# Performance work log

Measured on AMD Instinct MI355X. Metric: run time of the kernel, lower is better.

The kernel has to match this reference:

```python
import jax, jax.numpy as jnp
import numpy as np

N, IN_C, HID, OUT_C = 4096, 512, 512, 40
E = 131072
N_CLUSTERS, PCA_K, KMEANS_ITERS = 7, 10, 10
EPS = 1e-12


def _linear_params(key, fin, fout):
    k1, k2 = jax.random.split(key)
    lim = 1.0 / np.sqrt(fin)
    W = jax.random.uniform(k1, (fin, fout), jnp.float32, -lim, lim)
    b = jax.random.uniform(k2, (fout,), jnp.float32, -lim, lim)
    return W, b


def setup_inputs() -> dict:
    key = jax.random.key(0)
    ks = jax.random.split(key, 8)
    x = jax.random.normal(ks[0], (N, IN_C), jnp.float32)
    edge_index = jax.random.randint(ks[1], (2, E), 0, N, dtype=jnp.int32)
    y = jax.random.randint(ks[2], (N,), 0, N_CLUSTERS, dtype=jnp.int32)
    W_ego, b_ego = _linear_params(ks[3], IN_C, HID)
    W_cos, b_cos = _linear_params(ks[4], IN_C, HID)
    W_glob, b_glob = _linear_params(ks[5], IN_C, HID)
    W_fc, b_fc = _linear_params(ks[6], HID + IN_C + HID + HID, OUT_C)
    return dict(x=x, W_ego=W_ego, b_ego=b_ego, W_cos=W_cos, b_cos=b_cos,
                W_glob=W_glob, b_glob=b_glob, W_fc=W_fc, b_fc=b_fc,
                edge_index=edge_index, y=y)


def _mp_layer(x, W, b, src, dst):
    # MessagePassingLayer: scatter-add lin(x)[src] at dst, then relu
    h = x @ W + b
    agg = jax.ops.segment_sum(h[src], dst, num_segments=N)
    return jax.nn.relu(agg)


def _dominant_mask(x):
    # Dominant branch: PCA(10) -> KMeans(n_clusters) -> keep nodes with dist <= median.
    # sklearn's randomized KMeans replaced by deterministic Lloyd iterations
    # (init = first N_CLUSTERS rows); whole pipeline is detached in the original.
    xs = jax.lax.stop_gradient(x)
    xc = xs - xs.mean(0, keepdims=True)
    _, _, vt = jnp.linalg.svd(xc, full_matrices=False)
    feats = xc @ vt[:PCA_K].T  # [N, PCA_K]

    def step(c, _):
        d2 = ((feats[:, None, :] - c[None]) ** 2).sum(-1)  # [N, K]
        lab = jnp.argmin(d2, axis=1)
        sums = jax.ops.segment_sum(feats, lab, num_segments=N_CLUSTERS)
        cnt = jax.ops.segment_sum(jnp.ones((N,), jnp.float32), lab, num_segments=N_CLUSTERS)
        newc = jnp.where(cnt[:, None] > 0, sums / jnp.maximum(cnt, 1.0)[:, None], c)
        return newc, None

    centers, _ = jax.lax.scan(step, feats[:N_CLUSTERS], None, length=KMEANS_ITERS)
    d2 = ((feats[:, None, :] - centers[None]) ** 2).sum(-1)
    lab = jnp.argmin(d2, axis=1)
    dist = jnp.linalg.norm(feats - centers[lab], axis=1)
    keep = dist <= jnp.median(dist)
    return jax.lax.stop_gradient(keep.astype(jnp.float32))


def _forward(x, W_ego, b_ego, W_cos, b_cos, W_glob, b_glob, W_fc, b_fc, src, dst):
    # --- ego branch: exact 2-hop (source_to_target) subgraph mean per node ---
    # B[i, j] = 1 iff edge j->i; subset(i) = {i} | 1-hop | 2-hop (set semantics via >0)
    B = jnp.zeros((N, N), jnp.float32).at[dst, src].add(1.0)
    reach = jnp.eye(N, dtype=jnp.float32) + B + B @ B
    Mf = (reach > 0).astype(jnp.float32)
    ego_feats = (Mf @ x) / Mf.sum(1, keepdims=True)

    # --- Dominant branch: zero out far-from-center nodes ---
    keep = _dominant_mask(x)
    cut_enc = x * keep[:, None]

    # --- cosine branch: segment softmax over outgoing edges grouped by src ---
    norm_x = x / jnp.maximum(jnp.linalg.norm(x, axis=1, keepdims=True), EPS)
    sims = (norm_x[src] * norm_x[dst]).sum(-1)  # [E]
    smax = jax.ops.segment_max(sims, src, num_segments=N)
    ex = jnp.exp(sims - smax[src])
    den = jax.ops.segment_sum(ex, src, num_segments=N)
    w = ex / jnp.maximum(den, EPS)[src]
    num = jax.ops.segment_sum(w[:, None] * x[dst], src, num_segments=N)
    wsum = jax.ops.segment_sum(w, src, num_segments=N)
    deg = jax.ops.segment_sum(jnp.ones((E,), jnp.float32), src, num_segments=N)
    cos_feats = jnp.where(deg[:, None] > 0, num / jnp.maximum(wsum, EPS)[:, None], x)

    # --- encoders + head ---
    global_feats = x @ W_glob + b_glob
    ego_enc = _mp_layer(ego_feats, W_ego, b_ego, src, dst)
    cosine_enc = _mp_layer(cos_feats, W_cos, b_cos, src, dst)
    combined = jnp.concatenate([ego_enc, cut_enc, cosine_enc, global_feats], axis=-1)
    return jax.nn.log_softmax(combined @ W_fc + b_fc, axis=1)


def reference(x, W_ego, b_ego, W_cos, b_cos, W_glob, b_glob, W_fc, b_fc, edge_index, y):
    src, dst = edge_index[0], edge_index[1]
    return _forward(x, W_ego, b_ego, W_cos, b_cos, W_glob, b_glob, W_fc, b_fc, src, dst)
```

## Files before the change

### kernel.cpp

```cpp
#include <hip/hip_runtime.h>
#include <hip/hip_cooperative_groups.h>
#include <math.h>

namespace cg = cooperative_groups;

#define NN 4096
#define NC 512
#define NE 131072

typedef __bf16 bf16x8 __attribute__((ext_vector_type(8)));
typedef float f32x4 __attribute__((ext_vector_type(4)));
typedef unsigned short u16x8 __attribute__((ext_vector_type(8)));

__device__ __forceinline__ unsigned short f2b(float f){
  unsigned u = __float_as_uint(f);
  u += 0x7fffu + ((u >> 16) & 1u);
  return (unsigned short)(u >> 16);
}
__device__ __forceinline__ float b2f(unsigned short h){
  return __uint_as_float(((unsigned)h) << 16);
}
__device__ __forceinline__ float wredsum(float v){
  #pragma unroll
  for (int o = 32; o; o >>= 1) v += __shfl_xor(v, o, 64);
  return v;
}
__device__ __forceinline__ float wredmax(float v){
  #pragma unroll
  for (int o = 32; o; o >>= 1) v = fmaxf(v, __shfl_xor(v, o, 64));
  return v;
}

__global__ __launch_bounds__(256) void k_transconv(const float* __restrict__ src, int R, int C,
    unsigned short* __restrict__ dstT, int ldT, unsigned short* __restrict__ dstD){
  __shared__ unsigned short tile[64][65];
  int bc = blockIdx.x * 64, br = blockIdx.y * 64;
  int t = threadIdx.x, lc = t & 63, lr4 = t >> 6;
  for (int j = 0; j < 16; ++j){
    int r = br + lr4*16 + j, c = bc + lc;
    float v = (r < R && c < C) ? src[(size_t)r*C + c] : 0.f;
    unsigned short b = f2b(v);
    tile[lr4*16+j][lc] = b;
    if (dstD && r < R && c < C) dstD[(size_t)r*C + c] = b;
  }
  __syncthreads();
  for (int j = 0; j < 16; ++j){
    int cc = bc + lr4*16 + j, rr = br + lc;
    if (cc < C && rr < R) dstT[(size_t)cc*ldT + rr] = tile[lc][lr4*16+j];
  }
}

__global__ __launch_bounds__(256) void k_transconv3(const float* __restrict__ A,
    const float* __restrict__ B, const float* __restrict__ C,
    unsigned short* __restrict__ TA, unsigned short* __restrict__ TB, unsigned short* __restrict__ TC){
  __shared__ unsigned short tile[64][65];
  const float* src = (blockIdx.z == 0) ? A : ((blockIdx.z == 1) ? B : C);
  unsigned short* dstT = (blockIdx.z == 0) ? TA : ((blockIdx.z == 1) ? TB : TC);
  int bc = blockIdx.x * 64, br = blockIdx.y * 64;
  int t = threadIdx.x, lc = t & 63, lr4 = t >> 6;
  for (int j = 0; j < 16; ++j){
    int r = br + lr4*16 + j, c = bc + lc;
    tile[lr4*16+j][lc] = f2b(src[(size_t)r*512 + c]);
  }
  __syncthreads();
  for (int j = 0; j < 16; ++j){
    int cc = bc + lr4*16 + j, rr = br + lc;
    dstT[(size_t)cc*512 + rr] = tile[lc][lr4*16+j];
  }
}

__global__ __launch_bounds__(256) void k_normx(const float* __restrict__ x, unsigned short* __restrict__ nx){
  int wid = threadIdx.x >> 6, lane = threadIdx.x & 63;
  int row = blockIdx.x*4 + wid;
  const float* xr = x + (size_t)row*NC + lane*8;
  float v[8]; float ss = 0.f;
  #pragma unroll
  for (int j=0;j<8;j++){ v[j] = xr[j]; ss += v[j]*v[j]; }
  ss = wredsum(ss);
  float sc = 1.0f / fmaxf(sqrtf(ss), 1e-12f);
  u16x8 o;
  #pragma unroll
  for (int j=0;j<8;j++) o[j] = f2b(v[j]*sc);
  *(u16x8*)(nx + (size_t)row*NC + lane*8) = o;
}

__global__ void k_count_b1(const int* __restrict__ src, const int* __restrict__ dst,
    int* cin, int* cout, unsigned long long* B1){
  int e = blockIdx.x*256 + threadIdx.x;
  if (e < NE){
    int s = src[e], d = dst[e];
    atomicAdd(&cout[s], 1);
    atomicAdd(&cin[d], 1);
    atomicOr(&B1[(size_t)d*64 + (s>>6)], 1ull << (s & 63));
  }
}
__global__ __launch_bounds__(1024) void k_scan(const int* __restrict__ cnt0, const int* __restrict__ cnt1,
    int* off0, int* off1, int* fill0, int* fill1){
  __shared__ int s[1024];
  int t = threadIdx.x;
  for (int arr = 0; arr < 2; ++arr){
    const int* cnt = arr ? cnt1 : cnt0;
    int* off = arr ? off1 : off0;
    int* fill = arr ? fill1 : fill0;
    int a0 = cnt[t*4], a1 = cnt[t*4+1], a2 = cnt[t*4+2], a3 = cnt[t*4+3];
    int ts = a0+a1+a2+a3;
    s[t] = ts; __syncthreads();
    for (int o = 1; o < 1024; o <<= 1){
      int v = (t >= o) ? s[t-o] : 0; __syncthreads();
      s[t] += v; __syncthreads();
    }
    int ex = s[t] - ts;
    off[t*4] = ex; off[t*4+1] = ex+a0; off[t*4+2] = ex+a0+a1; off[t*4+3] = ex+a0+a1+a2;
    fill[t*4] = ex; fill[t*4+1] = ex+a0; fill[t*4+2] = ex+a0+a1; fill[t*4+3] = ex+a0+a1+a2;
    if (t == 1023) off[4096] = s[1023];
    __syncthreads();
  }
}
__global__ void k_fill(const int* __restrict__ src, const int* __restrict__ dst,
    int* fin, int* fout, int* csr_in, int* csr_out){
  int e = blockIdx.x*256 + threadIdx.x;
  if (e < NE){
    int s = src[e], d = dst[e];
    int pi = atomicAdd(&fin[d], 1);  csr_in[pi] = s;
    int po = atomicAdd(&fout[s], 1); csr_out[po] = d;
  }
}

__global__ __launch_bounds__(256) void k_bits2(const unsigned long long* __restrict__ B1,
    const int* __restrict__ off_in, const int* __restrict__ csr_in,
    unsigned short* __restrict__ Mf, float* __restrict__ rowrecip){
  int wid = threadIdx.x >> 6, lane = threadIdx.x & 63;
  int node = blockIdx.x*4 + wid;
  unsigned long long bits = B1[(size_t)node*64 + lane];
  if (lane == (node >> 6)) bits |= 1ull << (node & 63);
  int beg = off_in[node], end = off_in[node+1];
  for (int e = beg; e < end; ++e){
    int j = csr_in[e];
    bits |= B1[(size_t)j*64 + lane];
  }
  int pc = __popcll(bits);
  #pragma unroll
  for (int o = 32; o; o >>= 1) pc += __shfl_xor(pc, o, 64);
  if (lane == 0) rowrecip[node] = 1.0f / (float)pc;
  unsigned lo = (unsigned)(bits & 0xffffffffull), hi = (unsigned)(bits >> 32);
  unsigned int* Mrow = (unsigned int*)(Mf + (size_t)node*NN);
  for (int k = 0; k < 32; ++k){
    int srcl = 2*k + (lane >> 5);
    unsigned wlo = (unsigned)__shfl((int)lo, srcl, 64);
    unsigned whi = (unsigned)__shfl((int)hi, srcl, 64);
    unsigned long long w2 = ((unsigned long long)whi << 32) | wlo;
    int sh = (lane & 31) * 2;
    unsigned v = (unsigned)((w2 >> sh) & 3ull);
    Mrow[k*64 + lane] = ((v & 1u) ? 0x3F80u : 0u) | ((v & 2u) ? 0x3F800000u : 0u);
  }
}

template<int MODE>
__global__ __launch_bounds__(256) void gemm_bt(
    const unsigned short* __restrict__ A, int lda,
    const unsigned short* __restrict__ BT, int ldb,
    int K, int nstore,
    float* __restrict__ outF, unsigned short* __restrict__ outB, int ldc,
    const float* __restrict__ bias, const float* __restrict__ rowscale){
  __shared__ unsigned short Asm[64*40];
  __shared__ unsigned short Bsm[128*40];
  const int t = threadIdx.x;
  const int lane = t & 63, wid = t >> 6;
  const int wm = wid >> 1, wn = wid & 1;
  const int row0 = blockIdx.x * 64, col0 = blockIdx.y * 128;
  f32x4 acc[2][4];
  #pragma unroll
  for (int a = 0; a < 2; a++)
    #pragma unroll
    for (int b = 0; b < 4; b++){ acc[a][b][0]=0.f; acc[a][b][1]=0.f; acc[a][b][2]=0.f; acc[a][b][3]=0.f; }

  const int ar = t >> 2, as = t & 3;
  const unsigned short* Ap  = A  + (size_t)(row0 + ar)*lda + as*8;
  const unsigned short* Bp0 = BT + (size_t)(col0 + ar)*ldb + as*8;
  const unsigned short* Bp1 = BT + (size_t)(col0 + ar + 64)*ldb + as*8;
  unsigned short* Asd  = &Asm[ar*40 + as*8];
  unsigned short* Bsd0 = &Bsm[ar*40 + as*8];
  unsigned short* Bsd1 = &Bsm[(ar+64)*40 + as*8];

  const int fr = lane & 15, q = lane >> 4;
  const int aoff = (wm*32 + fr)*40 + q*8;
  const int boff = (wn*64 + fr)*40 + q*8;

  for (int k0 = 0; k0 < K; k0 += 32){
    *(u16x8*)Asd  = *(const u16x8*)(Ap  + k0);
    *(u16x8*)Bsd0 = *(const u16x8*)(Bp0 + k0);
    *(u16x8*)Bsd1 = *(const u16x8*)(Bp1 + k0);
    __syncthreads();
    bf16x8 af0 = *(const bf16x8*)&Asm[aoff];
    bf16x8 af1 = *(const bf16x8*)&Asm[aoff + 16*40];
    bf16x8 bfr[4];
    #pragma unroll
    for (int b = 0; b < 4; b++) bfr[b] = *(const bf16x8*)&Bsm[boff + b*16*40];
    #pragma unroll
    for (int b = 0; b < 4; b++){
      acc[0][b] = __builtin_amdgcn_mfma_f32_16x16x32_bf16(af0, bfr[b], acc[0][b], 0, 0, 0);
      acc[1][b] = __builtin_amdgcn_mfma_f32_16x16x32_bf16(af1, bfr[b], acc[1][b], 0, 0, 0);
    }
    __syncthreads();
  }
  #pragma unroll
  for (int a = 0; a < 2; a++){
    const int grow0 = row0 + wm*32 + a*16 + q*4;
    #pragma unroll
    for (int b = 0; b < 4; b++){
      const int gcol = col0 + wn*64 + b*16 + fr;
      if (gcol < nstore){
        #pragma unroll
        for (int r = 0; r < 4; r++){
          const int grow = grow0 + r;
          float v = acc[a][b][r];
          if (MODE == 0){ v *= rowscale[grow]; outB[(size_t)grow*ldc + gcol] = f2b(v); }
          if (MODE == 1){ v += bias[gcol];     outB[(size_t)grow*ldc + gcol] = f2b(v); }
          if (MODE == 2){ v += bias[gcol];     outF[(size_t)grow*ldc + gcol] = v; }
        }
      }
    }
  }
}

__global__ __launch_bounds__(256) void k_cos(const unsigned short* __restrict__ nx,
    const unsigned short* __restrict__ xb,
    const int* __restrict__ off_out, const int* __restrict__ csr_out,
    unsigned short* __restrict__ cosf){
  __shared__ float simsb[4][256];
  int wid = threadIdx.x >> 6, lane = threadIdx.x & 63;
  int node = blockIdx.x*4 + wid;
  float own[8];
  { u16x8 o = *(const u16x8*)(nx + (size_t)node*NC + lane*8);
    #pragma unroll
    for (int j=0;j<8;j++) own[j] = b2f(o[j]); }
  int beg = off_out[node], end = off_out[node+1], deg = end - beg;
  float m = -3.0e38f;
  for (int e = 0; e < deg; ++e){
    int d = csr_out[beg+e];
    u16x8 nb = *(const u16x8*)(nx + (size_t)d*NC + lane*8);
    float sp = 0.f;
    #pragma unroll
    for (int j=0;j<8;j++) sp += own[j]*b2f(nb[j]);
    float s = wredsum(sp);
    if (e < 256 && lane == 0) simsb[wid][e] = s;
    m = fmaxf(m, s);
  }
  float den = 0.f, acc[8] = {0,0,0,0,0,0,0,0};
  for (int e = 0; e < deg; ++e){
    int d = csr_out[beg+e];
    float s;
    if (e < 256) s = simsb[wid][e];
    else {
      u16x8 nb = *(const u16x8*)(nx + (size_t)d*NC + lane*8);
      float sp = 0.f;
      #pragma unroll
      for (int j=0;j<8;j++) sp += own[j]*b2f(nb[j]);
      s = wredsum(sp);
    }
    float w = expf(s - m);
    den += w;
    u16x8 xv = *(const u16x8*)(xb + (size_t)d*NC + lane*8);
    #pragma unroll
    for (int j=0;j<8;j++) acc[j] += w * b2f(xv[j]);
  }
  u16x8 o;
  if (deg > 0){
    float r = 1.0f/den;
    #pragma unroll
    for (int j=0;j<8;j++) o[j] = f2b(acc[j]*r);
  } else {
    o = *(const u16x8*)(xb + (size_t)node*NC + lane*8);
  }
  *(u16x8*)(cosf + (size_t)node*NC + lane*8) = o;
}

__global__ __launch_bounds__(256) void k_aggcut(const unsigned short* __restrict__ he,
    const unsigned short* __restrict__ hc,
    const int* __restrict__ off_in, const int* __restrict__ csr_in,
    const unsigned short* __restrict__ xb, const float* __restrict__ keep,
    unsigned short* __restrict__ comb){
  int wid = threadIdx.x >> 6, lane = threadIdx.x & 63;
  int node = blockIdx.x*4 + wid;
  float ae[8] = {0,0,0,0,0,0,0,0}, ac[8] = {0,0,0,0,0,0,0,0};
  int beg = off_in[node], end = off_in[node+1];
  for (int e = beg; e < end; ++e){
    int j = csr_in[e];
    u16x8 ve = *(const u16x8*)(he + (size_t)j*NC + lane*8);
    u16x8 vc = *(const u16x8*)(hc + (size_t)j*NC + lane*8);
    #pragma unroll
    for (int k=0;k<8;k++){ ae[k] += b2f(ve[k]); ac[k] += b2f(vc[k]); }
  }
  u16x8 oe, oc;
  #pragma unroll
  for (int k=0;k<8;k++){ oe[k] = f2b(fmaxf(ae[k], 0.f)); oc[k] = f2b(fmaxf(ac[k], 0.f)); }
  *(u16x8*)(comb + (size_t)node*2048 + lane*8) = oe;
  *(u16x8*)(comb + (size_t)node*2048 + 1024 + lane*8) = oc;
  u16x8 xv = *(const u16x8*)(xb + (size_t)node*NC + lane*8);
  if (keep[node] == 0.f){
    #pragma unroll
    for (int j=0;j<8;j++) xv[j] = 0;
  }
  *(u16x8*)(comb + (size_t)node*2048 + 512 + lane*8) = xv;
}

__global__ __launch_bounds__(256) void k_lsm(const float* __restrict__ logits, float* __restrict__ out){
  int wid = threadIdx.x >> 6, lane = threadIdx.x & 63;
  int row = blockIdx.x*4 + wid;
  float v = (lane < 40) ? logits[(size_t)row*64 + lane] : -3.0e38f;
  float m = wredmax(v);
  float e = (lane < 40) ? expf(v - m) : 0.f;
  float s = wredsum(e);
  float l = logf(s);
  if (lane < 40) out[(size_t)row*40 + lane] = v - m - l;
}

__global__ void k_colmean(const float* __restrict__ x, double* __restrict__ meanbuf){
  int c0 = threadIdx.x;
  int r0 = blockIdx.x*128;
  double s0 = 0, s1 = 0;
  for (int r = r0; r < r0+128; ++r){
    s0 += (double)x[(size_t)r*NC + c0];
    s1 += (double)x[(size_t)r*NC + c0 + 256];
  }
  atomicAdd(&meanbuf[c0], s0);
  atomicAdd(&meanbuf[c0+256], s1);
}

__global__ __launch_bounds__(256) void k_cov(const float* __restrict__ x,
    const double* __restrict__ meanbuf, double* __restrict__ Cm){
  __shared__ float sa[16][33];
  __shared__ float sb[16][33];
  const int t = threadIdx.x;
  const int ti = t & 15, tj = t >> 4;
  const int bi = blockIdx.x, bj = blockIdx.y;
  int l0 = t, l1 = t + 256;
  int r0a = l0 >> 5, c0a = l0 & 31;
  int r1a = l1 >> 5, c1a = l1 & 31;
  float ma0 = (float)(meanbuf[bi*32 + c0a] * (1.0/4096.0));
  float ma1 = (float)(meanbuf[bi*32 + c1a] * (1.0/4096.0));
  float mb0 = (float)(meanbuf[bj*32 + c0a] * (1.0/4096.0));
  float mb1 = (float)(meanbuf[bj*32 + c1a] * (1.0/4096.0));
  double a00=0,a01=0,a10=0,a11=0;
  for (int r0 = 0; r0 < NN; r0 += 16){
    sa[r0a][c0a] = x[(size_t)(r0 + r0a)*NC + bi*32 + c0a] - ma0;
    sa[r1a][c1a] = x[(size_t)(r0 + r1a)*NC + bi*32 + c1a] - ma1;
    sb[r0a][c0a] = x[(size_t)(r0 + r0a)*NC + bj*32 + c0a] - mb0;
    sb[r1a][c1a] = x[(size_t)(r0 + r1a)*NC + bj*32 + c1a] - mb1;
    __syncthreads();
    #pragma unroll
    for (int rr = 0; rr < 16; ++rr){
      double av0 = (double)sa[rr][ti], av1 = (double)sa[rr][ti+16];
      double bv0 = (double)sb[rr][tj], bv1 = (double)sb[rr][tj+16];
      a00 += av0*bv0; a01 += av0*bv1; a10 += av1*bv0; a11 += av1*bv1;
    }
    __syncthreads();
  }
  Cm[(size_t)(bi*32+ti)*512 + bj*32+tj]       = a00;
  Cm[(size_t)(bi*32+ti)*512 + bj*32+tj+16]    = a01;
  Cm[(size_t)(bi*32+ti+16)*512 + bj*32+tj]    = a10;
  Cm[(size_t)(bi*32+ti+16)*512 + bj*32+tj+16] = a11;
}

__global__ __launch_bounds__(256) void k_mm64(const double* __restrict__ A,
    const double* __restrict__ B, double* __restrict__ C){
  __shared__ double sa[32][17];
  __shared__ double sb[16][33];
  const int t = threadIdx.x;
  const int ti = t & 15, tj = t >> 4;
  const int bi = blockIdx.x, bj = blockIdx.y;
  double a00=0,a01=0,a10=0,a11=0;
  for (int k0 = 0; k0 < 512; k0 += 16){
    { int ii = t >> 4, kk = t & 15;
      sa[ii][kk] = A[(size_t)(bi*32+ii)*512 + k0+kk];
      int ii2 = (t+256) >> 4, kk2 = (t+256) & 15;
      sa[ii2][kk2] = A[(size_t)(bi*32+ii2)*512 + k0+kk2];
      int kk3 = t >> 5, jj3 = t & 31;
      sb[kk3][jj3] = B[(size_t)(k0+kk3)*512 + bj*32+jj3];
      int kk4 = (t+256) >> 5, jj4 = (t+256) & 31;
      sb[kk4][jj4] = B[(size_t)(k0+kk4)*512 + bj*32+jj4];
    }
    __syncthreads();
    #pragma unroll
    for (int kk = 0; kk < 16; ++kk){
      double av0 = sa[ti][kk], av1 = sa[ti+16][kk];
      double bv0 = sb[kk][tj], bv1 = sb[kk][tj+16];
      a00 += av0*bv0; a01 += av0*bv1; a10 += av1*bv0; a11 += av1*bv1;
    }
    __syncthreads();
  }
  C[(size_t)(bi*32+ti)*512 + bj*32+tj]       = a00;
  C[(size_t)(bi*32+ti)*512 + bj*32+tj+16]    = a01;
  C[(size_t)(bi*32+ti+16)*512 + bj*32+tj]    = a10;
  C[(size_t)(bi*32+ti+16)*512 + bj*32+tj+16] = a11;
}

union TailSmem {
  double red[256];
  double L[32][33];
  struct {
    double G[32][33], H[32][33], Q[32][33];
    double pcs[16], pss[16];
    int pp[16], pq[16], map[32], idx[10];
    double eig[32];
  } jac;
  struct {
    float cs[7][10];
    float fs[256][10];
    unsigned char labs[256];
    float sums[77];
  } km;
  struct {
    unsigned u[4096];
    int redc[4];
  } med;
};

__device__ __forceinline__ void matv_step(const double* __restrict__ M,
    const double* __restrict__ Vin, double* __restrict__ Vout, double scale, int gid){
  int r = gid >> 5, c = gid & 31;
  const double* Mr = M + (size_t)r*512;
  double s0=0,s1=0,s2=0,s3=0;
  for (int k = 0; k < 512; k += 4){
    s0 += Mr[k]   * Vin[(size_t)k*32 + c];
    s1 += Mr[k+1] * Vin[(size_t)(k+1)*32 + c];
    s2 += Mr[k+2] * Vin[(size_t)(k+2)*32 + c];
    s3 += Mr[k+3] * Vin[(size_t)(k+3)*32 + c];
  }
  Vout[gid] = ((s0+s1)+(s2+s3))*scale;
}

__global__ __launch_bounds__(256) void k_tail(
    const double* __restrict__ Cm, const double* __restrict__ C16m, const double* __restrict__ C64m,
    double* __restrict__ Va, double* __restrict__ Vb, double* __restrict__ Yb, double* __restrict__ Gm,
    const float* __restrict__ x, const double* __restrict__ meanbuf, float* __restrict__ Pm,
    float* __restrict__ feats, float* __restrict__ part2, float* __restrict__ distb,
    float* __restrict__ keep){
  cg::grid_group grid = cg::this_grid();
  __shared__ TailSmem sm;
  __shared__ double s_scal0, s_scal1;
  const int t = threadIdx.x;
  const int b = blockIdx.x;
  const int gid = b*256 + t;

  {
    double m0 = -1e300, m1 = -1e300;
    for (int i = t; i < 512; i += 256){
      m0 = fmax(m0, C16m[(size_t)i*512 + i]);
      m1 = fmax(m1, C64m[(size_t)i*512 + i]);
    }
    sm.red[t] = m0; __syncthreads();
    for (int o = 128; o; o >>= 1){ if (t < o) sm.red[t] = fmax(sm.red[t], sm.red[t+o]); __syncthreads(); }
    if (t == 0) s_scal0 = 1.0 / fmax(sm.red[0], 1e-300);
    __syncthreads();
    sm.red[t] = m1; __syncthreads();
    for (int o = 128; o; o >>= 1){ if (t < o) sm.red[t] = fmax(sm.red[t], sm.red[t+o]); __syncthreads(); }
    if (t == 0) s_scal1 = 1.0 / fmax(sm.red[0], 1e-300);
    __syncthreads();
  }

  {
    unsigned h = (unsigned)gid * 2654435761u + 12345u;
    h ^= h >> 13; h *= 2246822519u; h ^= h >> 16;
    Va[gid] = ((double)(h & 0xffffu) / 32768.0) - 1.0;
  }
  grid.sync();

  for (int it = 0; it < 2; ++it){
    matv_step(C64m, Va, Vb, s_scal1, gid);
    grid.sync();
    matv_step(C16m, Vb, Va, s_scal0, gid);
    grid.sync();
    if (t < 16){
      int e = b*16 + t; int i = e >> 5, j = e & 31;
      double s = 0;
      for (int k = 0; k < 512; ++k) s += Va[(size_t)k*32+i]*Va[(size_t)k*32+j];
      Gm[e] = s;
    }
    grid.sync();
    {
      for (int l = t; l < 1024; l += 256){ int i = l >> 5, j = l & 31; sm.L[i][j] = Gm[l]; }
      __syncthreads();
      for (int k = 0; k < 32; ++k){
        if (t == 0) sm.L[k][k] = sqrt(fmax(sm.L[k][k], 1e-300));
        __syncthreads();
        if (t > k && t < 32) sm.L[t][k] /= sm.L[k][k];
        __syncthreads();
        for (int l = t; l < 1024; l += 256){
          int i = l >> 5, j = l & 31;
          if (i > k && j > k && j <= i) sm.L[i][j] -= sm.L[i][k]*sm.L[j][k];
        }
        __syncthreads();
      }
      if (t < 8){
        int r = b*8 + t;
        double v[32];
        #pragma unroll
        for (int jj = 0; jj < 32; ++jj) v[jj] = Va[(size_t)r*32 + jj];
        #pragma unroll
        for (int jj = 0; jj < 32; ++jj){
          double s = v[jj];
          #pragma unroll
          for (int ii = 0; ii < 32; ++ii) if (ii < jj) s -= sm.L[jj][ii]*v[ii];
          v[jj] = s / sm.L[jj][jj];
        }
        #pragma unroll
        for (int jj = 0; jj < 32; ++jj) Va[(size_t)r*32 + jj] = v[jj];
      }
      __syncthreads();
    }
    grid.sync();
  }

  matv_step(Cm, Va, Yb, 1.0, gid);
  grid.sync();

  if (t < 16){
    int e = b*16 + t; int i = e >> 5, j = e & 31;
    double s = 0;
    for (int k = 0; k < 512; ++k) s += Va[(size_t)k*32+i]*Yb[(size_t)k*32+j];
    Gm[e] = s;
  }
  grid.sync();

  if (b == 0){
    for (int l = t; l < 1024; l += 256){
      int i = l >> 5, j = l & 31;
      sm.jac.G[i][j] = 0.5*(Gm[i*32+j] + Gm[j*32+i]);
      sm.jac.Q[i][j] = (i == j) ? 1.0 : 0.0;
    }
    __syncthreads();
    for (int sweep = 0; sweep < 6; ++sweep)
    for (int r = 0; r < 31; ++r){
      if (t < 16){
        int u = (t == 0) ? 0 : ((r + t - 1) % 31) + 1;
        int v = ((r + 30 - t) % 31) + 1;
        int p_ = u < v ? u : v, q_ = u < v ? v : u;
        double app = sm.jac.G[p_][p_], aqq = sm.jac.G[q_][q_], apq = sm.jac.G[p_][q_];
        double c, s;
        if (fabs(apq) < 1e-280){ c = 1.0; s = 0.0; }
        else {
          double tau = (aqq - app)/(2.0*apq);
          double tt = (tau >= 0 ? 1.0 : -1.0)/(fabs(tau) + sqrt(1.0 + tau*tau));
          c = 1.0/sqrt(1.0 + tt*tt); s = tt*c;
        }
        sm.jac.pcs[t] = c; sm.jac.pss[t] = s; sm.jac.pp[t] = p_; sm.jac.pq[t] = q_;
        sm.jac.map[p_] = t; sm.jac.map[q_] = t | 32;
      }
      __syncthreads();
      for (int l = t; l < 1024; l += 256){
        int i = l >> 5, j = l & 31;
        int mi = sm.jac.map[i], k = mi & 31;
        double c = sm.jac.pcs[k], s = sm.jac.pss[k];
        double gp = sm.jac.G[sm.jac.pp[k]][j], gq = sm.jac.G[sm.jac.pq[k]][j];
        sm.jac.H[i][j] = (mi & 32) ? (s*gp + c*gq) : (c*gp - s*gq);
      }
      __syncthreads();
      for (int l = t; l < 512; l += 256){
        int i = l >> 4, k = l & 15;
        double c = sm.jac.pcs[k], s = sm.jac.pss[k];
        int p_ = sm.jac.pp[k], q_ = sm.jac.pq[k];
        double hp = sm.jac.H[i][p_], hq = sm.jac.H[i][q_];
        sm.jac.G[i][p_] = c*hp - s*hq; sm.jac.G[i][q_] = s*hp + c*hq;
        double qp = sm.jac.Q[i][p_], qq = sm.jac.Q[i][q_];
        sm.jac.Q[i][p_] = c*qp - s*qq; sm.jac.Q[i][q_] = s*qp + c*qq;
      }
      __syncthreads();
    }
    if (t == 0){
      for (int i2 = 0; i2 < 32; ++i2) sm.jac.eig[i2] = sm.jac.G[i2][i2];
      unsigned used = 0;
      for (int k = 0; k < 10; ++k){
        int best = 0; double bv = -1e300;
        for (int i2 = 0; i2 < 32; ++i2)
          if (!((used >> i2) & 1u) && sm.jac.eig[i2] > bv){ bv = sm.jac.eig[i2]; best = i2; }
        used |= 1u << best; sm.jac.idx[k] = best;
      }
    }
    __syncthreads();
    for (int l = t; l < 5120; l += 256){
      int k = l/10, j = l%10;
      int c = sm.jac.idx[j];
      double s2 = 0;
      for (int m = 0; m < 32; ++m) s2 += Va[(size_t)k*32+m]*sm.jac.Q[m][c];
      Pm[k*10+j] = (float)s2;
    }
  }
  grid.sync();

  for (int id = gid; id < 65536; id += 16384){
    int n = id >> 4, j = id & 15;
    if (j < 10){
      float s = 0;
      for (int c2 = 0; c2 < 512; ++c2)
        s += (x[(size_t)n*512+c2] - (float)(meanbuf[c2]*(1.0/4096.0))) * Pm[c2*10+j];
      feats[n*10+j] = s;
    }
  }
  grid.sync();

  if (t < 70) sm.km.cs[t/10][t%10] = feats[t];
  if (b < 16){
    int base = b*256;
    for (int i = t; i < 2560; i += 256) sm.km.fs[i/10][i%10] = feats[base*10 + i];
  }
  __syncthreads();
  for (int iter = 0; iter < 10; ++iter){
    float* pbuf = part2 + (size_t)(iter & 1)*16*77;
    if (b < 16){
      float f[10];
      #pragma unroll
      for (int d = 0; d < 10; ++d) f[d] = sm.km.fs[t][d];
      int best = 0; float bd = 3.0e38f;
      for (int k = 0; k < 7; ++k){
        float s = 0;
        #pragma unroll
        for (int d = 0; d < 10; ++d){ float df = f[d]-sm.km.cs[k][d]; s += df*df; }
        if (s < bd){ bd = s; best = k; }
      }
      sm.km.labs[t] = (unsigned char)best;
      __syncthreads();
      if (t < 77){
        float acc = 0;
        if (t < 70){
          int k = t/10, d = t%10;
          for (int nn = 0; nn < 256; ++nn) if (sm.km.labs[nn] == k) acc += sm.km.fs[nn][d];
        } else {
          int k = t - 70;
          for (int nn = 0; nn < 256; ++nn) if (sm.km.labs[nn] == k) acc += 1.f;
        }
        pbuf[b*77 + t] = acc;
      }
    }
    grid.sync();
    if (t < 77){
      float s = 0;
      for (int bb = 0; bb < 16; ++bb) s += pbuf[bb*77 + t];
      sm.km.sums[t] = s;
    }
    __syncthreads();
    if (t < 70){
      float cnt = sm.km.sums[70 + t/10];
      if (cnt > 0.f) sm.km.cs[t/10][t%10] = sm.km.sums[t] / fmaxf(cnt, 1.f);
    }
    __syncthreads();
  }
  if (b < 16){
    float f[10];
    #pragma unroll
    for (int d = 0; d < 10; ++d) f[d] = sm.km.fs[t][d];
    float bd = 3.0e38f;
    for (int k = 0; k < 7; ++k){
      float s = 0;
      #pragma unroll
      for (int d = 0; d < 10; ++d){ float df = f[d]-sm.km.cs[k][d]; s += df*df; }
      bd = fminf(bd, s);
    }
    distb[b*256 + t] = sqrtf(bd);
  }
  grid.sync();

  if (b == 0){
    for (int i = t; i < 4096; i += 256) sm.med.u[i] = __float_as_uint(distb[i]);
    __syncthreads();
    unsigned vals[2];
    for (int ri = 0; ri < 2; ++ri){
      int r = 2047 + ri;
      unsigned prefix = 0;
      for (int bit = 31; bit >= 0; --bit){
        unsigned hm = (bit < 31) ? (0xffffffffu << (bit+1)) : 0u;
        int c = 0;
        for (int i = t; i < 4096; i += 256){
          unsigned e = sm.med.u[i];
          if ((e & hm) == prefix && !((e >> bit) & 1u)) c++;
        }
        #pragma unroll
        for (int o = 32; o; o >>= 1) c += __shfl_xor(c, o, 64);
        if ((t & 63) == 0) sm.med.redc[t >> 6] = c;
        __syncthreads();
        int tot = sm.med.redc[0] + sm.med.redc[1] + sm.med.redc[2] + sm.med.redc[3];
        if (r >= tot){ prefix |= (1u << bit); r -= tot; }
        __syncthreads();
      }
      vals[ri] = prefix;
    }
    float med = 0.5f*(__uint_as_float(vals[0]) + __uint_as_float(vals[1]));
    for (int i = t; i < 4096; i += 256) keep[i] = (distb[i] <= med) ? 1.f : 0.f;
  }
}

extern "C" void kernel_launch(void* const* d_in, const int* in_sizes, int n_in,
                              void* d_out, int out_size, void* d_ws, size_t ws_size,
                              hipStream_t stream){
  const float* x      = (const float*)d_in[0];
  const float* W_ego  = (const float*)d_in[1];
  const float* b_ego  = (const float*)d_in[2];
  const float* W_cos  = (const float*)d_in[3];
  const float* b_cos  = (const float*)d_in[4];
  const float* W_glob = (const float*)d_in[5];
  const float* b_glob = (const float*)d_in[6];
  const float* W_fc   = (const float*)d_in[7];
  const float* b_fc   = (const float*)d_in[8];
  const int*   ei     = (const int*)d_in[9];
  const int* src = ei;
  const int* dst = ei + NE;
  float* out = (float*)d_out;

  char* p = (char*)d_ws;
  auto alloc = [&](size_t n) -> char* { char* r = p; p += (n + 255) & ~(size_t)255; return r; };

  unsigned long long* B1 = (unsigned long long*)alloc((size_t)NN*64*8);
  unsigned short* Mf     = (unsigned short*)alloc((size_t)NN*NN*2);
  unsigned short* x_bf   = (unsigned short*)alloc((size_t)NN*NC*2);
  unsigned short* xT_bf  = (unsigned short*)alloc((size_t)NN*NC*2);
  unsigned short* nx_bf  = (unsigned short*)alloc((size_t)NN*NC*2);
  unsigned short* egof   = (unsigned short*)alloc((size_t)NN*NC*2);
  unsigned short* cosf   = (unsigned short*)alloc((size_t)NN*NC*2);
  unsigned short* h_ego  = (unsigned short*)alloc((size_t)NN*NC*2);
  unsigned short* h_cos  = (unsigned short*)alloc((size_t)NN*NC*2);
  unsigned short* WegoT  = (unsigned short*)alloc((size_t)512*512*2);
  unsigned short* WcosT  = (unsigned short*)alloc((size_t)512*512*2);
  unsigned short* WglobT = (unsigned short*)alloc((size_t)512*512*2);
  unsigned short* WfcT   = (unsigned short*)alloc((size_t)128*2048*2);
  unsigned short* comb   = (unsigned short*)alloc((size_t)NN*2048*2);
  float* logits   = (float*)alloc((size_t)NN*64*4);
  float* rowrecip = (float*)alloc((size_t)NN*4);
  float* keep     = (float*)alloc((size_t)NN*4);
  int* cnt_in   = (int*)alloc((size_t)NN*4);
  int* cnt_out  = (int*)alloc((size_t)NN*4);
  int* off_in   = (int*)alloc((size_t)(NN+1)*4);
  int* off_out  = (int*)alloc((size_t)(NN+1)*4);
  int* fill_in  = (int*)alloc((size_t)NN*4);
  int* fill_out = (int*)alloc((size_t)NN*4);
  int* csr_in   = (int*)alloc((size_t)NE*4);
  int* csr_out  = (int*)alloc((size_t)NE*4);
  double* meanbuf = (double*)alloc(512*8);
  double* Cm  = (double*)alloc((size_t)512*512*8);
  double* C2m = (double*)alloc((size_t)512*512*8);
  double* C4m = (double*)alloc((size_t)512*512*8);
  double* C8m = (double*)alloc((size_t)512*512*8);
  double* C16m = (double*)alloc((size_t)512*512*8);
  double* C32m = (double*)alloc((size_t)512*512*8);
  double* C64m = (double*)alloc((size_t)512*512*8);
  double* Va  = (double*)alloc((size_t)512*32*8);
  double* Vb  = (double*)alloc((size_t)512*32*8);
  double* Yb  = (double*)alloc((size_t)512*32*8);
  double* Gm  = (double*)alloc(32*32*8);
  float* Pm    = (float*)alloc((size_t)512*10*4);
  float* feats = (float*)alloc((size_t)NN*10*4);
  float* part  = (float*)alloc((size_t)2*16*77*4);
  float* distb = (float*)alloc((size_t)NN*4);

  hipMemsetAsync(B1, 0, (size_t)NN*64*8, stream);
  hipMemsetAsync(cnt_in, 0, (size_t)NN*4, stream);
  hipMemsetAsync(cnt_out, 0, (size_t)NN*4, stream);
  hipMemsetAsync(meanbuf, 0, 512*8, stream);
  hipMemsetAsync(WfcT, 0, (size_t)128*2048*2, stream);

  k_transconv<<<dim3(8,64), 256, 0, stream>>>(x, NN, NC, xT_bf, NN, x_bf);
  k_transconv3<<<dim3(8,8,3), 256, 0, stream>>>(W_ego, W_cos, W_glob, WegoT, WcosT, WglobT);
  k_transconv<<<dim3(1,32), 256, 0, stream>>>(W_fc, 2048, 40, WfcT, 2048, (unsigned short*)0);
  k_normx<<<1024, 256, 0, stream>>>(x, nx_bf);

  k_count_b1<<<512, 256, 0, stream>>>(src, dst, cnt_in, cnt_out, B1);
  k_scan<<<1, 1024, 0, stream>>>(cnt_in, cnt_out, off_in, off_out, fill_in, fill_out);
  k_fill<<<512, 256, 0, stream>>>(src, dst, fill_in, fill_out, csr_in, csr_out);
  k_bits2<<<1024, 256, 0, stream>>>(B1, off_in, csr_in, Mf, rowrecip);

  gemm_bt<0><<<dim3(64,4), 256, 0, stream>>>(Mf, NN, xT_bf, NN, NN, NC,
      (float*)0, egof, NC, (const float*)0, rowrecip);

  k_colmean<<<32, 256, 0, stream>>>(x, meanbuf);
  k_cov<<<dim3(16,16), 256, 0, stream>>>(x, meanbuf, Cm);
  k_mm64<<<dim3(16,16), 256, 0, stream>>>(Cm,  Cm,  C2m);
  k_mm64<<<dim3(16,16), 256, 0, stream>>>(C2m, C2m, C4m);
  k_mm64<<<dim3(16,16), 256, 0, stream>>>(C4m, C4m, C8m);
  k_mm64<<<dim3(16,16), 256, 0, stream>>>(C8m, C8m, C16m);
  k_mm64<<<dim3(16,16), 256, 0, stream>>>(C16m, C16m, C32m);
  k_mm64<<<dim3(16,16), 256, 0, stream>>>(C32m, C32m, C64m);

  {
    void* args[] = { (void*)&Cm, (void*)&C16m, (void*)&C64m, (void*)&Va, (void*)&Vb,
                     (void*)&Yb, (void*)&Gm, (void*)&x, (void*)&meanbuf, (void*)&Pm,
                     (void*)&feats, (void*)&part, (void*)&distb, (void*)&keep };
    hipLaunchCooperativeKernel((void*)k_tail, dim3(64), dim3(256), args, 0, stream);
  }

  k_cos<<<1024, 256, 0, stream>>>(nx_bf, x_bf, off_out, csr_out, cosf);

  gemm_bt<1><<<dim3(64,4), 256, 0, stream>>>(egof, NC, WegoT, 512, 512, NC,
      (float*)0, h_ego, NC, b_ego, (const float*)0);
  gemm_bt<1><<<dim3(64,4), 256, 0, stream>>>(cosf, NC, WcosT, 512, 512, NC,
      (float*)0, h_cos, NC, b_cos, (const float*)0);
  gemm_bt<1><<<dim3(64,4), 256, 0, stream>>>(x_bf, NC, WglobT, 512, 512, NC,
      (float*)0, comb + 1536, 2048, b_glob, (const float*)0);

  k_aggcut<<<1024, 256, 0, stream>>>(h_ego, h_cos, off_in, csr_in, x_bf, keep, comb);

  gemm_bt<2><<<dim3(64,1), 256, 0, stream>>>(comb, 2048, WfcT, 2048, 2048, 40,
      logits, (unsigned short*)0, 64, b_fc, (const float*)0);
  k_lsm<<<1024, 256, 0, stream>>>(logits, out);
}
```

Measured before the change: 1.826 ms.

## Exploit covariance symmetry, batch encoder GEMMs, and trim Jacobi sweeps

The covariance and repeated-squaring fp64 matmul kernels now compute only upper-triangle tiles and mirror-write them, roughly halving their work. The three encoder linear GEMMs are merged into one launch using blockIdx.z to select operands, which cuts launch count and fills more of the GPU. The Jacobi eigensolver sweep count drops from six to five, which shortens the serial tail but may reduce eigenvector accuracy.

```diff
diff --git a/kernel.cpp b/kernel.cpp
--- a/kernel.cpp
+++ b/kernel.cpp
@@ -223,6 +223,76 @@
   }
 }
 
+__global__ __launch_bounds__(256) void gemm_bt3(
+    const unsigned short* __restrict__ A0, const unsigned short* __restrict__ A1, const unsigned short* __restrict__ A2,
+    const unsigned short* __restrict__ B0, const unsigned short* __restrict__ B1g, const unsigned short* __restrict__ B2,
+    const float* __restrict__ bias0, const float* __restrict__ bias1, const float* __restrict__ bias2,
+    unsigned short* __restrict__ o0, unsigned short* __restrict__ o1, unsigned short* __restrict__ o2,
+    int ldc2){
+  const int z = blockIdx.z;
+  const unsigned short* A  = (z == 0) ? A0 : ((z == 1) ? A1 : A2);
+  const unsigned short* BT = (z == 0) ? B0 : ((z == 1) ? B1g : B2);
+  const float* bias        = (z == 0) ? bias0 : ((z == 1) ? bias1 : bias2);
+  unsigned short* outB     = (z == 0) ? o0 : ((z == 1) ? o1 : o2);
+  const int ldc = (z == 2) ? ldc2 : 512;
+
+  __shared__ unsigned short Asm[64*40];
+  __shared__ unsigned short Bsm[128*40];
+  const int t = threadIdx.x;
+  const int lane = t & 63, wid = t >> 6;
+  const int wm = wid >> 1, wn = wid & 1;
+  const int row0 = blockIdx.x * 64, col0 = blockIdx.y * 128;
+  f32x4 acc[2][4];
+  #pragma unroll
+  for (int a = 0; a < 2; a++)
+    #pragma unroll
+    for (int b = 0; b < 4; b++){ acc[a][b][0]=0.f; acc[a][b][1]=0.f; acc[a][b][2]=0.f; acc[a][b][3]=0.f; }
+
+  const int ar = t >> 2, as = t & 3;
+  const unsigned short* Ap  = A  + (size_t)(row0 + ar)*512 + as*8;
+  const unsigned short* Bp0 = BT + (size_t)(col0 + ar)*512 + as*8;
+  const unsigned short* Bp1 = BT + (size_t)(col0 + ar + 64)*512 + as*8;
+  unsigned short* Asd  = &Asm[ar*40 + as*8];
+  unsigned short* Bsd0 = &Bsm[ar*40 + as*8];
+  unsigned short* Bsd1 = &Bsm[(ar+64)*40 + as*8];
+
+  const int fr = lane & 15, q = lane >> 4;
+  const int aoff = (wm*32 + fr)*40 + q*8;
+  const int boff = (wn*64 + fr)*40 + q*8;
+
+  for (int k0 = 0; k0 < 512; k0 += 32){
+    *(u16x8*)Asd  = *(const u16x8*)(Ap  + k0);
+    *(u16x8*)Bsd0 = *(const u16x8*)(Bp0 + k0);
+    *(u16x8*)Bsd1 = *(const u16x8*)(Bp1 + k0);
+    __syncthreads();
+    bf16x8 af0 = *(const bf16x8*)&Asm[aoff];
+    bf16x8 af1 = *(const bf16x8*)&Asm[aoff + 16*40];
+    bf16x8 bfr[4];
+    #pragma unroll
+    for (int b = 0; b < 4; b++) bfr[b] = *(const bf16x8*)&Bsm[boff + b*16*40];
+    #pragma unroll
+    for (int b = 0; b < 4; b++){
+      acc[0][b] = __builtin_amdgcn_mfma_f32_16x16x32_bf16(af0, bfr[b], acc[0][b], 0, 0, 0);
+      acc[1][b] = __builtin_amdgcn_mfma_f32_16x16x32_bf16(af1, bfr[b], acc[1][b], 0, 0, 0);
+    }
+    __syncthreads();
+  }
+  #pragma unroll
+  for (int a = 0; a < 2; a++){
+    const int grow0 = row0 + wm*32 + a*16 + q*4;
+    #pragma unroll
+    for (int b = 0; b < 4; b++){
+      const int gcol = col0 + wn*64 + b*16 + fr;
+      #pragma unroll
+      for (int r = 0; r < 4; r++){
+        const int grow = grow0 + r;
+        float v = acc[a][b][r] + bias[gcol];
+        outB[(size_t)grow*ldc + gcol] = f2b(v);
+      }
+    }
+  }
+}
+
 __global__ __launch_bounds__(256) void k_cos(const unsigned short* __restrict__ nx,
     const unsigned short* __restrict__ xb,
     const int* __restrict__ off_out, const int* __restrict__ csr_out,
@@ -329,11 +399,12 @@
 
 __global__ __launch_bounds__(256) void k_cov(const float* __restrict__ x,
     const double* __restrict__ meanbuf, double* __restrict__ Cm){
+  const int bi = blockIdx.x, bj = blockIdx.y;
+  if (bi > bj) return;
   __shared__ float sa[16][33];
   __shared__ float sb[16][33];
   const int t = threadIdx.x;
   const int ti = t & 15, tj = t >> 4;
-  const int bi = blockIdx.x, bj = blockIdx.y;
   int l0 = t, l1 = t + 256;
   int r0a = l0 >> 5, c0a = l0 & 31;
   int r1a = l1 >> 5, c1a = l1 & 31;
@@ -356,19 +427,27 @@
     }
     __syncthreads();
   }
-  Cm[(size_t)(bi*32+ti)*512 + bj*32+tj]       = a00;
-  Cm[(size_t)(bi*32+ti)*512 + bj*32+tj+16]    = a01;
-  Cm[(size_t)(bi*32+ti+16)*512 + bj*32+tj]    = a10;
-  Cm[(size_t)(bi*32+ti+16)*512 + bj*32+tj+16] = a11;
+  const int r0i = bi*32+ti, r1i = bi*32+ti+16, c0j = bj*32+tj, c1j = bj*32+tj+16;
+  Cm[(size_t)r0i*512 + c0j] = a00;
+  Cm[(size_t)r0i*512 + c1j] = a01;
+  Cm[(size_t)r1i*512 + c0j] = a10;
+  Cm[(size_t)r1i*512 + c1j] = a11;
+  if (bi < bj){
+    Cm[(size_t)c0j*512 + r0i] = a00;
+    Cm[(size_t)c1j*512 + r0i] = a01;
+    Cm[(size_t)c0j*512 + r1i] = a10;
+    Cm[(size_t)c1j*512 + r1i] = a11;
+  }
 }
 
 __global__ __launch_bounds__(256) void k_mm64(const double* __restrict__ A,
     const double* __restrict__ B, double* __restrict__ C){
+  const int bi = blockIdx.x, bj = blockIdx.y;
+  if (bi > bj) return;
   __shared__ double sa[32][17];
   __shared__ double sb[16][33];
   const int t = threadIdx.x;
   const int ti = t & 15, tj = t >> 4;
-  const int bi = blockIdx.x, bj = blockIdx.y;
   double a00=0,a01=0,a10=0,a11=0;
   for (int k0 = 0; k0 < 512; k0 += 16){
     { int ii = t >> 4, kk = t & 15;
@@ -389,10 +468,17 @@
     }
     __syncthreads();
   }
-  C[(size_t)(bi*32+ti)*512 + bj*32+tj]       = a00;
-  C[(size_t)(bi*32+ti)*512 + bj*32+tj+16]    = a01;
-  C[(size_t)(bi*32+ti+16)*512 + bj*32+tj]    = a10;
-  C[(size_t)(bi*32+ti+16)*512 + bj*32+tj+16] = a11;
+  const int r0i = bi*32+ti, r1i = bi*32+ti+16, c0j = bj*32+tj, c1j = bj*32+tj+16;
+  C[(size_t)r0i*512 + c0j] = a00;
+  C[(size_t)r0i*512 + c1j] = a01;
+  C[(size_t)r1i*512 + c0j] = a10;
+  C[(size_t)r1i*512 + c1j] = a11;
+  if (bi < bj){
+    C[(size_t)c0j*512 + r0i] = a00;
+    C[(size_t)c1j*512 + r0i] = a01;
+    C[(size_t)c0j*512 + r1i] = a10;
+    C[(size_t)c1j*512 + r1i] = a11;
+  }
 }
 
 union TailSmem {
@@ -530,7 +616,7 @@
       sm.jac.Q[i][j] = (i == j) ? 1.0 : 0.0;
     }
     __syncthreads();
-    for (int sweep = 0; sweep < 6; ++sweep)
+    for (int sweep = 0; sweep < 5; ++sweep)
     for (int r = 0; r < 31; ++r){
       if (t < 16){
         int u = (t == 0) ? 0 : ((r + t - 1) % 31) + 1;
@@ -788,12 +874,12 @@
 
   k_cos<<<1024, 256, 0, stream>>>(nx_bf, x_bf, off_out, csr_out, cosf);
 
-  gemm_bt<1><<<dim3(64,4), 256, 0, stream>>>(egof, NC, WegoT, 512, 512, NC,
-      (float*)0, h_ego, NC, b_ego, (const float*)0);
-  gemm_bt<1><<<dim3(64,4), 256, 0, stream>>>(cosf, NC, WcosT, 512, 512, NC,
-      (float*)0, h_cos, NC, b_cos, (const float*)0);
-  gemm_bt<1><<<dim3(64,4), 256, 0, stream>>>(x_bf, NC, WglobT, 512, 512, NC,
-      (float*)0, comb + 1536, 2048, b_glob, (const float*)0);
+  gemm_bt3<<<dim3(64,4,3), 256, 0, stream>>>(
+      egof, cosf, x_bf,
+      WegoT, WcosT, WglobT,
+      b_ego, b_cos, b_glob,
+      h_ego, h_cos, comb + 1536,
+      2048);
 
   k_aggcut<<<1024, 256, 0, stream>>>(h_ego, h_cos, off_in, csr_in, x_bf, keep, comb);
 
```

Result: faster. 1.762 ms (-3.5%).
